# Optimization experiments

Hardware: AMD Instinct MI355X
Metric: run time of the kernel (lower is better)

## Reference

```python
import jax, jax.numpy as jnp
import numpy as np

C = 256          # in_channels == inter_channels (structurally required)
B, H, W = 16, 64, 64


def setup_inputs() -> dict:
    key = jax.random.key(0)
    ks = jax.random.split(key, 10)
    s = 1.0 / np.sqrt(C)
    x = jax.random.normal(ks[0], (B, C, H, W), dtype=jnp.float32)
    # theta / phi: 1x1 convs, stored as [out, in]
    theta_w = jax.random.normal(ks[1], (C, C), dtype=jnp.float32) * s
    theta_b = jax.random.normal(ks[2], (C,), dtype=jnp.float32) * s
    phi_w = jax.random.normal(ks[3], (C, C), dtype=jnp.float32) * s
    phi_b = jax.random.normal(ks[4], (C,), dtype=jnp.float32) * s
    # grouped conv: Conv2d(C, 2C, kernel=(C,1), groups=C).
    # torch weight [2C, 1, C, 1] with group-major out-channel order -> [C groups, 2 per group, C taps]
    gw = jax.random.normal(ks[5], (C, 2, C), dtype=jnp.float32) * s
    gb = jax.random.normal(ks[6], (C, 2), dtype=jnp.float32) * s
    # dim_adjust: 1x1 conv 2C -> C, stored as [C, 2C]
    dw = jax.random.normal(ks[7], (C, 2 * C), dtype=jnp.float32) * (1.0 / np.sqrt(2 * C))
    db = jax.random.normal(ks[8], (C,), dtype=jnp.float32) * (1.0 / np.sqrt(2 * C))
    return {"x": x, "theta_w": theta_w, "theta_b": theta_b,
            "phi_w": phi_w, "phi_b": phi_b,
            "gw": gw, "gb": gb, "dw": dw, "db": db}


def reference(x, theta_w, theta_b, phi_w, phi_b, gw, gb, dw, db):
    b, c, h, w = x.shape
    xf = x.reshape(b, c, h * w)                                   # [B,C,HW]
    theta = jnp.einsum('oc,bcn->bon', theta_w, xf) + theta_b[:, None]  # [B,Ci,HW]
    phi = jnp.einsum('oc,bcn->bon', phi_w, xf) + phi_b[:, None]        # [B,Ci,HW]
    f = jnp.einsum('bon,bpn->bop', theta, phi)                    # [B,Ci,Ci] channel similarity
    # grouped conv: group g sees channel g of f over its 'spatial' axis (length Ci),
    # producing 2 outputs per group via a full-height dot product.
    g = jnp.einsum('bgk,gjk->bgj', f, gw) + gb                    # [B,C,2]
    g = jax.nn.relu(g).reshape(b, 2 * c)                          # [B,2C]
    out = jnp.einsum('bo,co->bc', g, dw) + db                     # [B,C] 1x1 conv
    return out[:, :, None, None]                                  # [B,C,1,1]
```

## Files before the change

kernel.cpp:

```cpp
#include <hip/hip_runtime.h>


#define CC  256
#define NB  16
#define HWN 4096
#define KSPLIT 32
#define NPAIR 136

typedef __attribute__((ext_vector_type(4))) float f32x4;
typedef __attribute__((ext_vector_type(8))) short bf16x8;

__device__ inline unsigned short f2bf(float f) {
  unsigned u = __float_as_uint(f);
  u += 0x7fff + ((u >> 16) & 1);
  return (unsigned short)(u >> 16);
}
__device__ inline float bf2f(unsigned u) { return __uint_as_float(u << 16); }

__global__ __launch_bounds__(1024, 4) void k_gram(const float* __restrict__ x,
                                                  unsigned short* __restrict__ slab,
                                                  float* __restrict__ Spart) {
  const int ks = blockIdx.x, b = blockIdx.y;
  const float* xb = x + (size_t)b * CC * HWN;
  __shared__ unsigned short As[2][256 * 64];

  const int tid = threadIdx.x, w = tid >> 6, lane = tid & 63;
  const int quad = lane >> 4, m15 = lane & 15;
  const int srow = tid >> 4;
  const int scol = (tid & 15) << 2;
  const int sg = scol >> 3, so = scol & 7;

  f32x4 acc[16];
  #pragma unroll
  for (int i = 0; i < 16; ++i) acc[i] = (f32x4){0.f, 0.f, 0.f, 0.f};
  float rs[4] = {0.f, 0.f, 0.f, 0.f};

  const int k0 = ks * 128;
  float4 ld[4];
  #pragma unroll
  for (int p = 0; p < 4; ++p)
    ld[p] = *(const float4*)(xb + (size_t)(p * 64 + srow) * HWN + k0 + scol);
  #pragma unroll
  for (int p = 0; p < 4; ++p) {
    const int row = p * 64 + srow;
    rs[p] += ld[p].x + ld[p].y + ld[p].z + ld[p].w;
    *(ushort4*)&As[0][row * 64 + ((sg ^ (row & 7)) << 3) + so] =
        make_ushort4(f2bf(ld[p].x), f2bf(ld[p].y), f2bf(ld[p].z), f2bf(ld[p].w));
  }
  __syncthreads();

  #pragma unroll
  for (int i = 0; i < 2; ++i) {
    if (i < 1) {
      #pragma unroll
      for (int p = 0; p < 4; ++p)
        ld[p] = *(const float4*)(xb + (size_t)(p * 64 + srow) * HWN + k0 + 64 + scol);
    }
    const int rowa = 16 * w + m15;
    #pragma unroll
    for (int kkg = 0; kkg < 8; kkg += 4) {
      const int ga = (kkg + quad) ^ (m15 & 7);
      bf16x8 af = *(const bf16x8*)&As[i][rowa * 64 + ga * 8];
      #pragma unroll
      for (int ct = 0; ct < 16; ++ct) {
        if (ct < w) continue;
        bf16x8 bfr = *(const bf16x8*)&As[i][(16 * ct + m15) * 64 + ga * 8];
        acc[ct] = __builtin_amdgcn_mfma_f32_16x16x32_bf16(af, bfr, acc[ct], 0, 0, 0);
      }
    }
    if (i < 1) {
      #pragma unroll
      for (int p = 0; p < 4; ++p) {
        const int row = p * 64 + srow;
        rs[p] += ld[p].x + ld[p].y + ld[p].z + ld[p].w;
        *(ushort4*)&As[1][row * 64 + ((sg ^ (row & 7)) << 3) + so] =
            make_ushort4(f2bf(ld[p].x), f2bf(ld[p].y), f2bf(ld[p].z), f2bf(ld[p].w));
      }
    }
    __syncthreads();
  }

  const int off_w = 16 * w - (w * (w - 1)) / 2;
  unsigned short* sbase = slab + ((size_t)(ks * 16 + b) * NPAIR) * 256;
  #pragma unroll
  for (int ct = 0; ct < 16; ++ct) {
    if (ct < w) continue;
    const int pid = off_w + (ct - w);
    uint2 ov;
    ov.x = (unsigned)f2bf(acc[ct][0]) | ((unsigned)f2bf(acc[ct][1]) << 16);
    ov.y = (unsigned)f2bf(acc[ct][2]) | ((unsigned)f2bf(acc[ct][3]) << 16);
    *(uint2*)(sbase + pid * 256 + lane * 4) = ov;
  }

  #pragma unroll
  for (int p = 0; p < 4; ++p) {
    float v = rs[p];
    v += __shfl_xor(v, 1);
    v += __shfl_xor(v, 2);
    v += __shfl_xor(v, 4);
    v += __shfl_xor(v, 8);
    if ((tid & 15) == 0)
      Spart[(ks * 16 + b) * 256 + p * 64 + srow] = v;
  }
}

__global__ __launch_bounds__(256) void k_fuse1(const unsigned short* __restrict__ slab,
                                               const float* __restrict__ Spart,
                                               const float* __restrict__ gw,
                                               const float* __restrict__ pw,
                                               const float* __restrict__ pb,
                                               const float* __restrict__ tw,
                                               unsigned short* __restrict__ Gh,
                                               unsigned short* __restrict__ Qh,
                                               float* __restrict__ E,
                                               float* __restrict__ U,
                                               float* __restrict__ V) {
  const int blk = blockIdx.x, tid = threadIdx.x;
  if (blk < 544) {
    const int t = blk * 256 + tid;
    const int b = t / 8704;
    const int rem = t % 8704;
    const int pid0 = rem >> 6, lane = rem & 63;
    int w = 0, p = pid0;
    while (p >= 16 - w) { p -= 16 - w; ++w; }
    const int ct = w + p;
    const int quad = lane >> 4, m15 = lane & 15;
    float s[4] = {0.f, 0.f, 0.f, 0.f};
    const unsigned short* sp = slab + (size_t)(b * NPAIR + pid0) * 256 + lane * 4;
    #pragma unroll
    for (int ks = 0; ks < KSPLIT; ++ks) {
      const uint2 v = *(const uint2*)(sp + (size_t)ks * 16 * NPAIR * 256);
      s[0] += bf2f(v.x & 0xffffu); s[1] += bf2f(v.x >> 16);
      s[2] += bf2f(v.y & 0xffffu); s[3] += bf2f(v.y >> 16);
    }
    unsigned short h[4];
    #pragma unroll
    for (int r = 0; r < 4; ++r) h[r] = f2bf(s[r]);
    unsigned short* Gb = Gh + ((size_t)b << 16);
    const int rb = 16 * w + quad * 4;
    const int col = 16 * ct + m15;
    #pragma unroll
    for (int r = 0; r < 4; ++r) Gb[(rb + r) * 256 + col] = h[r];
    uint2 mv;
    mv.x = (unsigned)h[0] | ((unsigned)h[1] << 16);
    mv.y = (unsigned)h[2] | ((unsigned)h[3] << 16);
    *(uint2*)(Gb + col * 256 + rb) = mv;
  } else if (blk < 1056) {
    const int rj = blk - 544;
    __shared__ float sm[512];
    sm[tid] = gw[rj * 256 + tid];
    __syncthreads();
    float q = 0.f;
    for (int p = 0; p < 256; ++p) q += sm[p] * pw[p * 256 + tid];
    Qh[rj * 256 + tid] = f2bf(q);
    sm[256 + tid] = sm[tid] * pb[tid];
    __syncthreads();
    for (int s = 128; s > 0; s >>= 1) {
      if (tid < s) sm[256 + tid] += sm[256 + tid + s];
      __syncthreads();
    }
    if (tid == 0) E[rj] = sm[256];
  } else {
    const int m = blk - 1056;
    const int b = m & 15, mat = m >> 4;
    const float* Wm = mat ? pw : tw;
    float* outp = mat ? V : U;
    __shared__ float sm[256];
    float sv = 0.f;
    #pragma unroll
    for (int ks = 0; ks < KSPLIT; ++ks)
      sv += Spart[(ks * 16 + b) * 256 + tid];
    sm[tid] = sv;
    __syncthreads();
    const int l = tid & 15, oh = tid >> 4;
    #pragma unroll
    for (int oc = 0; oc < 16; ++oc) {
      const int o = oc * 16 + oh;
      float a = 0.f;
      #pragma unroll
      for (int j = 0; j < 16; ++j)
        a += Wm[o * 256 + l * 16 + j] * sm[l * 16 + j];
      a += __shfl_xor(a, 1);
      a += __shfl_xor(a, 2);
      a += __shfl_xor(a, 4);
      a += __shfl_xor(a, 8);
      if (l == 0) outp[b * 256 + o] = a;
    }
  }
}

__global__ __launch_bounds__(256) void k_p(const unsigned short* __restrict__ Gh,
                                           const unsigned short* __restrict__ Qh,
                                           const float* __restrict__ tw,
                                           const float* __restrict__ gw,
                                           const float* __restrict__ U,
                                           const float* __restrict__ V,
                                           const float* __restrict__ E,
                                           const float* __restrict__ tb,
                                           const float* __restrict__ gb,
                                           float* __restrict__ GR) {
  const int rjt = blockIdx.x, b = blockIdx.y;
  const int rj0 = rjt * 16;
  const int tid = threadIdx.x, w = tid >> 6, lane = tid & 63;
  const int quad = lane >> 4, m15 = lane & 15;
  const unsigned short* Gb = Gh + ((size_t)b << 16);

  f32x4 acc[4];
  #pragma unroll
  for (int mt = 0; mt < 4; ++mt) acc[mt] = (f32x4){0.f, 0.f, 0.f, 0.f};

  #pragma unroll
  for (int s = 0; s < 8; ++s) {
    const int kb = s * 32 + quad * 8;
    bf16x8 bq = *(const bf16x8*)(Qh + (rj0 + m15) * 256 + kb);
    #pragma unroll
    for (int mt = 0; mt < 4; ++mt) {
      bf16x8 ag = *(const bf16x8*)(Gb + (64 * w + 16 * mt + m15) * 256 + kb);
      acc[mt] = __builtin_amdgcn_mfma_f32_16x16x32_bf16(ag, bq, acc[mt], 0, 0, 0);
    }
  }

  __shared__ float sred[16 * 4];
  __shared__ float sred2[16];
  {
    const int rj = rj0 + m15;
    const int r = rj >> 1;
    float p = 0.f;
    #pragma unroll
    for (int mt = 0; mt < 4; ++mt)
      #pragma unroll
      for (int reg = 0; reg < 4; ++reg)
        p += acc[mt][reg] * tw[r * 256 + 64 * w + 16 * mt + quad * 4 + reg];
    p += __shfl_xor(p, 16);
    p += __shfl_xor(p, 32);
    if (quad == 0) sred[m15 * 4 + w] = p;
  }
  {
    const int oi = tid >> 4, seg = tid & 15;
    const int rj = rj0 + oi;
    float p2 = 0.f;
    #pragma unroll
    for (int i = 0; i < 16; ++i) {
      const int cp = seg * 16 + i;
      p2 += gw[rj * 256 + cp] * V[b * 256 + cp];
    }
    p2 += __shfl_xor(p2, 1);
    p2 += __shfl_xor(p2, 2);
    p2 += __shfl_xor(p2, 4);
    p2 += __shfl_xor(p2, 8);
    if (seg == 0) sred2[oi] = p2;
  }
  __syncthreads();
  if (tid < 16) {
    const int rj = rj0 + tid, r = rj >> 1;
    const float v = sred[tid * 4] + sred[tid * 4 + 1] +
                    sred[tid * 4 + 2] + sred[tid * 4 + 3];
    const float tbr = tb[r];
    const float bias = tbr * sred2[tid] +
                       (U[b * 256 + r] + 4096.0f * tbr) * E[rj] + gb[rj];
    GR[b * 512 + rj] = fmaxf(v + bias, 0.f);
  }
}

__global__ __launch_bounds__(256) void k_out(const float* __restrict__ GR,
                                             const float* __restrict__ dw,
                                             const float* __restrict__ db,
                                             float* __restrict__ out) {
  const int cch = blockIdx.x, b = blockIdx.y, tid = threadIdx.x;
  __shared__ float gl[512];
  gl[tid] = GR[b * 512 + tid];
  gl[256 + tid] = GR[b * 512 + 256 + tid];
  __syncthreads();
  const int cl = tid >> 4, l = tid & 15;
  const int c = cch * 16 + cl;
  float a = 0.f;
  #pragma unroll 8
  for (int i = 0; i < 32; ++i) {
    const int o = i * 16 + l;
    a += gl[o] * dw[c * 512 + o];
  }
  a += __shfl_xor(a, 1);
  a += __shfl_xor(a, 2);
  a += __shfl_xor(a, 4);
  a += __shfl_xor(a, 8);
  if (l == 0) out[b * 256 + c] = a + db[c];
}

extern "C" void kernel_launch(void* const* d_in, const int* in_sizes, int n_in,
                              void* d_out, int out_size, void* d_ws, size_t ws_size,
                              hipStream_t stream) {
  const float* x  = (const float*)d_in[0];
  const float* tw = (const float*)d_in[1];
  const float* tb = (const float*)d_in[2];
  const float* pw = (const float*)d_in[3];
  const float* pb = (const float*)d_in[4];
  const float* gw = (const float*)d_in[5];
  const float* gb = (const float*)d_in[6];
  const float* dw = (const float*)d_in[7];
  const float* db = (const float*)d_in[8];
  float* out = (float*)d_out;

  unsigned short* slab = (unsigned short*)d_ws;
  unsigned short* Gh   = slab + (size_t)KSPLIT * 16 * NPAIR * 256;
  unsigned short* Qh   = Gh + ((size_t)16 << 16);
  float* Spart = (float*)(Qh + 512 * 256);
  float* E  = Spart + KSPLIT * 16 * 256;
  float* U  = E + 512;
  float* V  = U + NB * 256;
  float* GR = V + NB * 256;

  k_gram<<<dim3(KSPLIT, 16), 1024, 0, stream>>>(x, slab, Spart);
  k_fuse1<<<1088, 256, 0, stream>>>(slab, Spart, gw, pw, pb, tw, Gh, Qh, E, U, V);
  k_p<<<dim3(32, NB), 256, 0, stream>>>(Gh, Qh, tw, gw, U, V, E, tb, gb, GR);
  k_out<<<dim3(16, NB), 256, 0, stream>>>(GR, dw, db, out);
}
```

Measured before the change: 152.2 us.

## Fold Q/E precompute into gram kernel and fuse output projection via atomics

Moves the weight-only Q=gw·pw and E precompute out of the second kernel and into extra blocks of the gram kernel, so it runs alongside the x streaming. The final dim_adjust projection is folded into k_p: each block applies its 16 relu outputs to the matching columns of dw and atomically adds into out, which k_fuse2 pre-initialises with the bias. This removes one kernel launch and the GR round trip, in exchange for float atomics (non-deterministic summation order) and an uncoalesced strided read of dw in k_p. Launch bounds for the gram kernel are also raised.

Result: slower. 219.0 us (+43.9%).

```diff
diff --git a/kernel.cpp b/kernel.cpp
--- a/kernel.cpp
+++ b/kernel.cpp
@@ -17,14 +17,40 @@
 }
 __device__ inline float bf2f(unsigned u) { return __uint_as_float(u << 16); }
 
-__global__ __launch_bounds__(1024, 4) void k_gram(const float* __restrict__ x,
+__global__ __launch_bounds__(1024, 8) void k_gram(const float* __restrict__ x,
                                                   unsigned short* __restrict__ slab,
-                                                  float* __restrict__ Spart) {
-  const int ks = blockIdx.x, b = blockIdx.y;
+                                                  float* __restrict__ Spart,
+                                                  const float* __restrict__ gw,
+                                                  const float* __restrict__ pw,
+                                                  const float* __restrict__ pb,
+                                                  unsigned short* __restrict__ Qh,
+                                                  float* __restrict__ E) {
+  __shared__ __align__(16) unsigned short As[2][256 * 64];
+  const int blk = blockIdx.x, tid = threadIdx.x;
+
+  if (blk >= 512) {
+    const int sub = tid >> 8, t = tid & 255;
+    const int rj = (blk - 512) * 4 + sub;
+    float* smg = (float*)As + sub * 512;
+    smg[t] = gw[rj * 256 + t];
+    __syncthreads();
+    float q = 0.f;
+    for (int p = 0; p < 256; ++p) q += smg[p] * pw[p * 256 + t];
+    Qh[rj * 256 + t] = f2bf(q);
+    smg[256 + t] = smg[t] * pb[t];
+    __syncthreads();
+    for (int s = 128; s > 0; s >>= 1) {
+      if (t < s) smg[256 + t] += smg[256 + t + s];
+      __syncthreads();
+    }
+    if (t == 0) E[rj] = smg[256];
+    return;
+  }
+
+  const int ks = blk >> 4, b = blk & 15;
   const float* xb = x + (size_t)b * CC * HWN;
-  __shared__ unsigned short As[2][256 * 64];
-
-  const int tid = threadIdx.x, w = tid >> 6, lane = tid & 63;
+
+  const int w = tid >> 6, lane = tid & 63;
   const int quad = lane >> 4, m15 = lane & 15;
   const int srow = tid >> 4;
   const int scol = (tid & 15) << 2;
@@ -104,17 +130,15 @@
   }
 }
 
-__global__ __launch_bounds__(256) void k_fuse1(const unsigned short* __restrict__ slab,
+__global__ __launch_bounds__(256) void k_fuse2(const unsigned short* __restrict__ slab,
                                                const float* __restrict__ Spart,
-                                               const float* __restrict__ gw,
                                                const float* __restrict__ pw,
-                                               const float* __restrict__ pb,
                                                const float* __restrict__ tw,
+                                               const float* __restrict__ db,
                                                unsigned short* __restrict__ Gh,
-                                               unsigned short* __restrict__ Qh,
-                                               float* __restrict__ E,
                                                float* __restrict__ U,
-                                               float* __restrict__ V) {
+                                               float* __restrict__ V,
+                                               float* __restrict__ out) {
   const int blk = blockIdx.x, tid = threadIdx.x;
   if (blk < 544) {
     const int t = blk * 256 + tid;
@@ -145,23 +169,8 @@
     mv.x = (unsigned)h[0] | ((unsigned)h[1] << 16);
     mv.y = (unsigned)h[2] | ((unsigned)h[3] << 16);
     *(uint2*)(Gb + col * 256 + rb) = mv;
-  } else if (blk < 1056) {
-    const int rj = blk - 544;
-    __shared__ float sm[512];
-    sm[tid] = gw[rj * 256 + tid];
-    __syncthreads();
-    float q = 0.f;
-    for (int p = 0; p < 256; ++p) q += sm[p] * pw[p * 256 + tid];
-    Qh[rj * 256 + tid] = f2bf(q);
-    sm[256 + tid] = sm[tid] * pb[tid];
-    __syncthreads();
-    for (int s = 128; s > 0; s >>= 1) {
-      if (tid < s) sm[256 + tid] += sm[256 + tid + s];
-      __syncthreads();
-    }
-    if (tid == 0) E[rj] = sm[256];
-  } else {
-    const int m = blk - 1056;
+  } else if (blk < 576) {
+    const int m = blk - 544;
     const int b = m & 15, mat = m >> 4;
     const float* Wm = mat ? pw : tw;
     float* outp = mat ? V : U;
@@ -186,6 +195,9 @@
       a += __shfl_xor(a, 8);
       if (l == 0) outp[b * 256 + o] = a;
     }
+  } else {
+    const int b = blk - 576;
+    out[b * 256 + tid] = db[tid];
   }
 }
 
@@ -198,7 +210,8 @@
                                            const float* __restrict__ E,
                                            const float* __restrict__ tb,
                                            const float* __restrict__ gb,
-                                           float* __restrict__ GR) {
+                                           const float* __restrict__ dw,
+                                           float* __restrict__ out) {
   const int rjt = blockIdx.x, b = blockIdx.y;
   const int rj0 = rjt * 16;
   const int tid = threadIdx.x, w = tid >> 6, lane = tid & 63;
@@ -222,6 +235,7 @@
 
   __shared__ float sred[16 * 4];
   __shared__ float sred2[16];
+  __shared__ float gsh[16];
   {
     const int rj = rj0 + m15;
     const int r = rj >> 1;
@@ -258,32 +272,14 @@
     const float tbr = tb[r];
     const float bias = tbr * sred2[tid] +
                        (U[b * 256 + r] + 4096.0f * tbr) * E[rj] + gb[rj];
-    GR[b * 512 + rj] = fmaxf(v + bias, 0.f);
-  }
-}
-
-__global__ __launch_bounds__(256) void k_out(const float* __restrict__ GR,
-                                             const float* __restrict__ dw,
-                                             const float* __restrict__ db,
-                                             float* __restrict__ out) {
-  const int cch = blockIdx.x, b = blockIdx.y, tid = threadIdx.x;
-  __shared__ float gl[512];
-  gl[tid] = GR[b * 512 + tid];
-  gl[256 + tid] = GR[b * 512 + 256 + tid];
+    gsh[tid] = fmaxf(v + bias, 0.f);
+  }
   __syncthreads();
-  const int cl = tid >> 4, l = tid & 15;
-  const int c = cch * 16 + cl;
   float a = 0.f;
-  #pragma unroll 8
-  for (int i = 0; i < 32; ++i) {
-    const int o = i * 16 + l;
-    a += gl[o] * dw[c * 512 + o];
-  }
-  a += __shfl_xor(a, 1);
-  a += __shfl_xor(a, 2);
-  a += __shfl_xor(a, 4);
-  a += __shfl_xor(a, 8);
-  if (l == 0) out[b * 256 + c] = a + db[c];
+  #pragma unroll
+  for (int i = 0; i < 16; ++i)
+    a += gsh[i] * dw[tid * 512 + rj0 + i];
+  atomicAdd(&out[b * 256 + tid], a);
 }
 
 extern "C" void kernel_launch(void* const* d_in, const int* in_sizes, int n_in,
@@ -307,10 +303,8 @@
   float* E  = Spart + KSPLIT * 16 * 256;
   float* U  = E + 512;
   float* V  = U + NB * 256;
-  float* GR = V + NB * 256;
-
-  k_gram<<<dim3(KSPLIT, 16), 1024, 0, stream>>>(x, slab, Spart);
-  k_fuse1<<<1088, 256, 0, stream>>>(slab, Spart, gw, pw, pb, tw, Gh, Qh, E, U, V);
-  k_p<<<dim3(32, NB), 256, 0, stream>>>(Gh, Qh, tw, gw, U, V, E, tb, gb, GR);
-  k_out<<<dim3(16, NB), 256, 0, stream>>>(GR, dw, db, out);
-}
+
+  k_gram<<<640, 1024, 0, stream>>>(x, slab, Spart, gw, pw, pb, Qh, E);
+  k_fuse2<<<592, 256, 0, stream>>>(slab, Spart, pw, tw, db, Gh, U, V, out);
+  k_p<<<dim3(32, NB), 256, 0, stream>>>(Gh, Qh, tw, gw, U, V, E, tb, gb, dw, out);
+}
```
